# Kernel optimization log

Measured on AMD Instinct MI355X. Metric: run time of the kernel, lower is better.

Reference implementation:

```python
import jax, jax.numpy as jnp
import numpy as np

# Canonical DAG: L topological levels of N nodes each; every node in level l>0
# has K predecessors in level l-1, each edge carrying a scalar weight.
# Input nodes (level 0) take x columns directly (no activation), matching the
# torch module. Output = activations of the (sorted) last-level nodes.

B, N, K, L = 1024, 5000, 16, 10  # batch, nodes/level, fan-in, levels
NEG_SLOPE = 0.1                  # LeakyReLU(0.1) as in the module


def setup_inputs() -> dict:
    key = jax.random.key(0)
    k_x, k_s, k_w, k_b = jax.random.split(key, 4)
    x = jax.random.normal(k_x, (B, N), dtype=jnp.float32)
    # predecessor indices into the previous level, per level 1..L-1
    src_idx = jax.random.randint(k_s, (L - 1, N, K), 0, N)
    # scalar edge weights and node biases ~ N(0, 0.1), as in __init__
    weights = jax.random.normal(k_w, (L - 1, N, K), dtype=jnp.float32) * 0.1
    biases = jax.random.normal(k_b, (L - 1, N), dtype=jnp.float32) * 0.1
    return {"x": x, "src_idx": src_idx, "weights": weights, "biases": biases}


def reference(x, src_idx, weights, biases):
    b, n = x.shape
    k = src_idx.shape[-1]

    def level(act, params):
        s, w, bias = params  # s,w: [N,K], bias: [N]
        # gather predecessor activations: [B, N, K]
        gathered = jnp.take(act, s.reshape(-1), axis=1).reshape(b, n, k)
        # weighted sum over predecessors + bias, then LeakyReLU(0.1)
        pre = jnp.einsum('bnk,nk->bn', gathered, w) + bias
        return jax.nn.leaky_relu(pre, NEG_SLOPE), None

    out, _ = jax.lax.scan(level, x, (src_idx, weights, biases))
    return out  # [B, N] activations of output nodes (sorted order)
```

## Files before the change

kernel.cpp:

```cpp
#include <hip/hip_runtime.h>


#define TB 1024
#define TN 5000
#define TK 16
#define TLV 9
#define CPG 4
#define NG  (TB / CPG)
#define LT  1024
#define PEL (TN * TK)

typedef unsigned int u32;
typedef unsigned short u16;
typedef _Float16 h2 __attribute__((ext_vector_type(2)));

__device__ __forceinline__ h2 u2h(u32 v) { return __builtin_bit_cast(h2, v); }
__device__ __forceinline__ u32 h2u(h2 h) { return __builtin_bit_cast(u32, h); }
__device__ __forceinline__ u32 packf(float a, float b) {
    h2 h; h.x = (_Float16)a; h.y = (_Float16)b;
    return h2u(h);
}

__global__ __launch_bounds__(256) void k_pack(
    const int* __restrict__ idx, const float* __restrict__ w,
    u32* __restrict__ pe)
{
    const int j = blockIdx.x * 256 + threadIdx.x;
    if (j < TLV * TN * TK) {
        const u32 s = (u32)idx[j];
        h2 hw; hw.x = (_Float16)w[j]; hw.y = (_Float16)0.0f;
        pe[j] = (s * 8u) | (h2u(hw) << 16);
    }
}

__global__ __launch_bounds__(LT) void k_fused(
    const float* __restrict__ x,
    float* __restrict__ out,
    const u32* __restrict__ pe,
    const float* __restrict__ biases)
{
    __shared__ uint2 buf[2][TN];
    const int g = blockIdx.x;
    const int t = threadIdx.x;

    {
        const float* xp0 = x + (size_t)(g * CPG + 0) * TN;
        const float* xp1 = x + (size_t)(g * CPG + 1) * TN;
        const float* xp2 = x + (size_t)(g * CPG + 2) * TN;
        const float* xp3 = x + (size_t)(g * CPG + 3) * TN;
        for (int n = t; n < TN; n += LT) {
            uint2 v;
            v.x = packf(xp0[n], xp1[n]);
            v.y = packf(xp2[n], xp3[n]);
            buf[0][n] = v;
        }
    }
    __syncthreads();

    int cur = 0;
    for (int l = 0; l < TLV; ++l) {
        const u32*   ep_l = pe + (size_t)l * PEL;
        const float* b_l  = biases + (size_t)l * TN;
        const char*  base = reinterpret_cast<const char*>(buf[cur]);
        for (int n = t; n < TN; n += LT) {
            const uint4* ep = reinterpret_cast<const uint4*>(ep_l + (size_t)n * TK);
            const uint4 e0 = ep[0];
            const uint4 e1 = ep[1];
            const uint4 e2 = ep[2];
            const uint4 e3 = ep[3];
            const u32 es[TK] = {e0.x, e0.y, e0.z, e0.w,
                                e1.x, e1.y, e1.z, e1.w,
                                e2.x, e2.y, e2.z, e2.w,
                                e3.x, e3.y, e3.z, e3.w};

            const float bvf = b_l[n];
            h2 bb; bb.x = (_Float16)bvf; bb.y = (_Float16)bvf;
            h2 a01 = bb, a23 = bb;

            #pragma unroll
            for (int k = 0; k < TK; ++k) {
                const u32 e   = es[k];
                const u32 off = e & 0xffffu;
                const h2 w2 = u2h(__builtin_amdgcn_perm(e, e, 0x03020302u));
                const uint2 av = *reinterpret_cast<const uint2*>(base + off);
                a01 = w2 * u2h(av.x) + a01;
                a23 = w2 * u2h(av.y) + a23;
            }

            h2 tenth; tenth.x = (_Float16)0.1f; tenth.y = (_Float16)0.1f;
            a01 = __builtin_elementwise_max(a01, a01 * tenth);
            a23 = __builtin_elementwise_max(a23, a23 * tenth);

            uint2 r; r.x = h2u(a01); r.y = h2u(a23);
            buf[cur ^ 1][n] = r;
        }
        __syncthreads();
        cur ^= 1;
    }

    {
        float* op0 = out + (size_t)(g * CPG + 0) * TN;
        float* op1 = out + (size_t)(g * CPG + 1) * TN;
        float* op2 = out + (size_t)(g * CPG + 2) * TN;
        float* op3 = out + (size_t)(g * CPG + 3) * TN;
        for (int n = t; n < TN; n += LT) {
            const uint2 v = buf[cur][n];
            h2 h;
            h = u2h(v.x); op0[n] = (float)h.x; op1[n] = (float)h.y;
            h = u2h(v.y); op2[n] = (float)h.x; op3[n] = (float)h.y;
        }
    }
}

extern "C" void kernel_launch(void* const* d_in, const int* in_sizes, int n_in,
                              void* d_out, int out_size, void* d_ws, size_t ws_size,
                              hipStream_t stream)
{
    const float* x       = (const float*)d_in[0];
    const int*   src_idx = (const int*)  d_in[1];
    const float* weights = (const float*)d_in[2];
    const float* biases  = (const float*)d_in[3];
    float* out = (float*)d_out;

    u32* pe = (u32*)d_ws;

    {
        const int ne = TLV * TN * TK;
        hipLaunchKernelGGL(k_pack, dim3((ne + 255) / 256), dim3(256), 0, stream,
                           src_idx, weights, pe);
    }
    hipLaunchKernelGGL(k_fused, dim3(NG), dim3(LT), 0, stream,
                       x, out, pe, biases);
}
```

Measured before the change: 128.9 us.

## Duplicate activations into permuted LDS copy and reorder edges to cut bank conflicts

Each level's activations are now written twice into LDS: once in natural order and once in a permuted slot layout (sigma). The pack kernel assigns each node's 16 edges to the slot order k so that the address at iteration k tends to fall on a distinct bank phase across lanes, choosing between the two copies. The aim is to reduce LDS bank conflicts in the random gather, and the FMA now uses inline v_pk_fma_f16 with op_sel to read the weight straight from the packed word without a perm. In exchange, LDS use doubles (about 160KB per block) and every level does two stores per node.

```diff
diff --git a/kernel.cpp b/kernel.cpp
--- a/kernel.cpp
+++ b/kernel.cpp
@@ -10,6 +10,9 @@
 #define LT  1024
 #define PEL (TN * TK)
 
+#define SLOTS_A 5008
+#define SLOTS   10016
+
 typedef unsigned int u32;
 typedef unsigned short u16;
 typedef _Float16 h2 __attribute__((ext_vector_type(2)));
@@ -20,17 +23,61 @@
     h2 h; h.x = (_Float16)a; h.y = (_Float16)b;
     return h2u(h);
 }
+__device__ __forceinline__ u32 sigma(u32 n) { return (n & 15u) * 313u + (n >> 4); }
 
-__global__ __launch_bounds__(256) void k_pack(
+__global__ __launch_bounds__(256) void k_pack2(
     const int* __restrict__ idx, const float* __restrict__ w,
     u32* __restrict__ pe)
 {
-    const int j = blockIdx.x * 256 + threadIdx.x;
-    if (j < TLV * TN * TK) {
-        const u32 s = (u32)idx[j];
-        h2 hw; hw.x = (_Float16)w[j]; hw.y = (_Float16)0.0f;
-        pe[j] = (s * 8u) | (h2u(hw) << 16);
+    __shared__ u32 asg[256][17];
+    const int t = threadIdx.x;
+    const int j = blockIdx.x * 256 + t;
+    const int NT = TLV * TN;
+
+    if (j < NT) {
+        const u32 n  = (u32)(j % TN);
+        const int eb = j * TK;
+        const int4*   ip = reinterpret_cast<const int4*>(idx + eb);
+        const float4* wp = reinterpret_cast<const float4*>(w + eb);
+        const int4   i0 = ip[0], i1 = ip[1], i2 = ip[2], i3 = ip[3];
+        const float4 w0 = wp[0], w1 = wp[1], w2 = wp[2], w3 = wp[3];
+        const int   si[TK] = {i0.x,i0.y,i0.z,i0.w, i1.x,i1.y,i1.z,i1.w,
+                              i2.x,i2.y,i2.z,i2.w, i3.x,i3.y,i3.z,i3.w};
+        const float wv[TK] = {w0.x,w0.y,w0.z,w0.w, w1.x,w1.y,w1.z,w1.w,
+                              w2.x,w2.y,w2.z,w2.w, w3.x,w3.y,w3.z,w3.w};
+
+        u32 used = 0, pendmask = 0;
+        u32 valA[TK];
+        #pragma unroll
+        for (int k = 0; k < TK; ++k) {
+            const u32 s = (u32)si[k];
+            h2 hw; hw.x = (_Float16)wv[k]; hw.y = (_Float16)0.0f;
+            const u32 wb = h2u(hw) << 16;
+            const u32 offA = s;
+            const u32 offB = SLOTS_A + sigma(s);
+            valA[k] = offA | wb;
+            const u32 kA = (offA - n) & 15u;
+            const u32 kB = (offB - n) & 15u;
+            if (!((used >> kA) & 1u))      { used |= 1u << kA; asg[t][kA] = offA | wb; }
+            else if (!((used >> kB) & 1u)) { used |= 1u << kB; asg[t][kB] = offB | wb; }
+            else pendmask |= 1u << k;
+        }
+        #pragma unroll
+        for (int k = 0; k < TK; ++k) {
+            if ((pendmask >> k) & 1u) {
+                const u32 slot = (u32)__builtin_ctz(~used);
+                used |= 1u << slot;
+                asg[t][slot] = valA[k];
+            }
+        }
     }
+    __syncthreads();
+
+    const int jb    = blockIdx.x * 256;
+    const int nodeN = min(256, NT - jb);
+    const int elems = nodeN * TK;
+    for (int p = t; p < elems; p += 256)
+        pe[(size_t)jb * TK + p] = asg[p >> 4][p & 15];
 }
 
 __global__ __launch_bounds__(LT) void k_fused(
@@ -39,7 +86,7 @@
     const u32* __restrict__ pe,
     const float* __restrict__ biases)
 {
-    __shared__ uint2 buf[2][TN];
+    __shared__ uint2 buf[2][SLOTS];
     const int g = blockIdx.x;
     const int t = threadIdx.x;
 
@@ -53,6 +100,7 @@
             v.x = packf(xp0[n], xp1[n]);
             v.y = packf(xp2[n], xp3[n]);
             buf[0][n] = v;
+            buf[0][SLOTS_A + sigma((u32)n)] = v;
         }
     }
     __syncthreads();
@@ -62,6 +110,7 @@
         const u32*   ep_l = pe + (size_t)l * PEL;
         const float* b_l  = biases + (size_t)l * TN;
         const char*  base = reinterpret_cast<const char*>(buf[cur]);
+        uint2* wb = buf[cur ^ 1];
         for (int n = t; n < TN; n += LT) {
             const uint4* ep = reinterpret_cast<const uint4*>(ep_l + (size_t)n * TK);
             const uint4 e0 = ep[0];
@@ -74,25 +123,28 @@
                                 e3.x, e3.y, e3.z, e3.w};
 
             const float bvf = b_l[n];
-            h2 bb; bb.x = (_Float16)bvf; bb.y = (_Float16)bvf;
-            h2 a01 = bb, a23 = bb;
+            u32 a01 = packf(bvf, bvf);
+            u32 a23 = a01;
 
             #pragma unroll
             for (int k = 0; k < TK; ++k) {
                 const u32 e   = es[k];
-                const u32 off = e & 0xffffu;
-                const h2 w2 = u2h(__builtin_amdgcn_perm(e, e, 0x03020302u));
+                const u32 off = (e & 0xffffu) << 3;
                 const uint2 av = *reinterpret_cast<const uint2*>(base + off);
-                a01 = w2 * u2h(av.x) + a01;
-                a23 = w2 * u2h(av.y) + a23;
+                asm("v_pk_fma_f16 %0, %1, %2, %0 op_sel:[1,0,0] op_sel_hi:[1,1,1]"
+                    : "+v"(a01) : "v"(e), "v"(av.x));
+                asm("v_pk_fma_f16 %0, %1, %2, %0 op_sel:[1,0,0] op_sel_hi:[1,1,1]"
+                    : "+v"(a23) : "v"(e), "v"(av.y));
             }
 
+            h2 A = u2h(a01), Bv = u2h(a23);
             h2 tenth; tenth.x = (_Float16)0.1f; tenth.y = (_Float16)0.1f;
-            a01 = __builtin_elementwise_max(a01, a01 * tenth);
-            a23 = __builtin_elementwise_max(a23, a23 * tenth);
+            A  = __builtin_elementwise_max(A,  A  * tenth);
+            Bv = __builtin_elementwise_max(Bv, Bv * tenth);
 
-            uint2 r; r.x = h2u(a01); r.y = h2u(a23);
-            buf[cur ^ 1][n] = r;
+            uint2 r; r.x = h2u(A); r.y = h2u(Bv);
+            wb[n] = r;
+            wb[SLOTS_A + sigma((u32)n)] = r;
         }
         __syncthreads();
         cur ^= 1;
@@ -125,8 +177,8 @@
     u32* pe = (u32*)d_ws;
 
     {
-        const int ne = TLV * TN * TK;
-        hipLaunchKernelGGL(k_pack, dim3((ne + 255) / 256), dim3(256), 0, stream,
+        const int nn = TLV * TN;
+        hipLaunchKernelGGL(k_pack2, dim3((nn + 255) / 256), dim3(256), 0, stream,
                            src_idx, weights, pe);
     }
     hipLaunchKernelGGL(k_fused, dim3(NG), dim3(LT), 0, stream,
```

Result: no change. 130.3 us (+1.1%).

## Software-pipeline edge prefetch across nodes and levels with inline packed FMA

Applied to the files above, without the earlier changes.

Unrolls the per-level node loop into fixed iterations that use two register sets, so the edge descriptors and bias for the next node (and the first node of the next level) are loaded while the current node is computed. The bias is pre-packed to half2 in the pack kernel. Edge indices now encode a ping-pong slot offset into one flat LDS array, so no per-level base pointer is needed. Inline v_pk_fma_f16 with op_sel takes the weight straight from the high half of the edge word, replacing the perm. Register pressure rises with two prefetch sets at 1024 threads, and the hardcoded slot/iteration layout depends on N=5000.

```diff
diff --git a/kernel.cpp b/kernel.cpp
--- a/kernel.cpp
+++ b/kernel.cpp
@@ -9,6 +9,10 @@
 #define NG  (TB / CPG)
 #define LT  1024
 #define PEL (TN * TK)
+
+#define SLOTP 5056
+#define PSTRIDE (SLOTP * 8)
+#define WOFF_IT 8192
 
 typedef unsigned int u32;
 typedef unsigned short u16;
@@ -23,88 +27,129 @@
 
 __global__ __launch_bounds__(256) void k_pack(
     const int* __restrict__ idx, const float* __restrict__ w,
-    u32* __restrict__ pe)
+    const float* __restrict__ biases,
+    u32* __restrict__ pe, u32* __restrict__ b2)
 {
     const int j = blockIdx.x * 256 + threadIdx.x;
     if (j < TLV * TN * TK) {
+        const int l = j / (TN * TK);
         const u32 s = (u32)idx[j];
         h2 hw; hw.x = (_Float16)w[j]; hw.y = (_Float16)0.0f;
-        pe[j] = (s * 8u) | (h2u(hw) << 16);
+        pe[j] = ((u32)(l & 1) * (u32)SLOTP + s) | (h2u(hw) << 16);
+    }
+    if (j < TLV * TN) {
+        const float b = biases[j];
+        b2[j] = packf(b, b);
     }
 }
+
+
+#define PREF(S, LL, IT) do {                                                  \
+    const size_t _n = (size_t)(LL) * TN + (size_t)(t + (IT) * LT);            \
+    const uint4* _p = reinterpret_cast<const uint4*>(pe + _n * TK);           \
+    S##a = _p[0]; S##b = _p[1]; S##c = _p[2]; S##d = _p[3];                   \
+    S##i = b2[_n];                                                            \
+} while (0)
+
+#define EDGE(EV) do {                                                         \
+    const u32 _e   = (EV);                                                    \
+    const u32 _off = (_e & 0xffffu) << 3;              \
+    const uint2 _av = *reinterpret_cast<const uint2*>(lds + _off);            \
+    asm("v_pk_fma_f16 %0, %1, %2, %0 op_sel:[1,0,0] op_sel_hi:[1,1,1]"        \
+        : "+v"(a01) : "v"(_e), "v"(_av.x));                                   \
+    asm("v_pk_fma_f16 %0, %1, %2, %0 op_sel:[1,0,0] op_sel_hi:[1,1,1]"        \
+        : "+v"(a23) : "v"(_e), "v"(_av.y));                                   \
+} while (0)
+
+#define COMP(S, WBASE, IT) do {                                               \
+    u32 a01 = S##i, a23 = S##i;                      \
+    EDGE(S##a.x); EDGE(S##a.y); EDGE(S##a.z); EDGE(S##a.w);                   \
+    EDGE(S##b.x); EDGE(S##b.y); EDGE(S##b.z); EDGE(S##b.w);                   \
+    EDGE(S##c.x); EDGE(S##c.y); EDGE(S##c.z); EDGE(S##c.w);                   \
+    EDGE(S##d.x); EDGE(S##d.y); EDGE(S##d.z); EDGE(S##d.w);                   \
+    h2 A = u2h(a01), Bv = u2h(a23);                                           \
+    h2 tenth; tenth.x = (_Float16)0.1f; tenth.y = (_Float16)0.1f;             \
+    A  = __builtin_elementwise_max(A,  A  * tenth);                           \
+    Bv = __builtin_elementwise_max(Bv, Bv * tenth);                           \
+    uint2 _r; _r.x = h2u(A); _r.y = h2u(Bv);                                  \
+    *reinterpret_cast<uint2*>(lds + (WBASE) + (IT) * WOFF_IT) = _r;           \
+} while (0)
+
+#define LVL(LL, S0, S1, WBASE, LAST) do {                                     \
+    PREF(S1, (LL), 1); COMP(S0, WBASE, 0);                                    \
+    PREF(S0, (LL), 2); COMP(S1, WBASE, 1);                                    \
+    PREF(S1, (LL), 3); COMP(S0, WBASE, 2);                                    \
+    if (t4) PREF(S0, (LL), 4);                                                \
+    COMP(S1, WBASE, 3);                                                       \
+    if (!(LAST)) PREF(S1, (LL) + 1, 0);                                       \
+    if (t4) COMP(S0, WBASE, 4);                                               \
+    __syncthreads();                                                          \
+} while (0)
 
 __global__ __launch_bounds__(LT) void k_fused(
     const float* __restrict__ x,
     float* __restrict__ out,
     const u32* __restrict__ pe,
-    const float* __restrict__ biases)
+    const u32* __restrict__ b2)
 {
-    __shared__ uint2 buf[2][TN];
+    __shared__ char lds[2 * PSTRIDE];
     const int g = blockIdx.x;
     const int t = threadIdx.x;
+    const bool t4 = t < (TN - 4 * LT);
+    const u32 woO = (u32)t * 8u;
+    const u32 woE = (u32)(SLOTP + t) * 8u;
+
+    uint4 Pa, Pb, Pc, Pd; u32 Pi;
+    uint4 Qa, Qb, Qc, Qd; u32 Qi;
+
+    PREF(P, 0, 0);
 
     {
         const float* xp0 = x + (size_t)(g * CPG + 0) * TN;
         const float* xp1 = x + (size_t)(g * CPG + 1) * TN;
         const float* xp2 = x + (size_t)(g * CPG + 2) * TN;
         const float* xp3 = x + (size_t)(g * CPG + 3) * TN;
-        for (int n = t; n < TN; n += LT) {
+        #pragma unroll
+        for (int it = 0; it < 4; ++it) {
+            const int n = t + it * LT;
             uint2 v;
             v.x = packf(xp0[n], xp1[n]);
             v.y = packf(xp2[n], xp3[n]);
-            buf[0][n] = v;
+            *reinterpret_cast<uint2*>(lds + woO + it * WOFF_IT) = v;
+        }
+        if (t4) {
+            const int n = t + 4 * LT;
+            uint2 v;
+            v.x = packf(xp0[n], xp1[n]);
+            v.y = packf(xp2[n], xp3[n]);
+            *reinterpret_cast<uint2*>(lds + woO + 4 * WOFF_IT) = v;
         }
     }
     __syncthreads();
 
-    int cur = 0;
-    for (int l = 0; l < TLV; ++l) {
-        const u32*   ep_l = pe + (size_t)l * PEL;
-        const float* b_l  = biases + (size_t)l * TN;
-        const char*  base = reinterpret_cast<const char*>(buf[cur]);
-        for (int n = t; n < TN; n += LT) {
-            const uint4* ep = reinterpret_cast<const uint4*>(ep_l + (size_t)n * TK);
-            const uint4 e0 = ep[0];
-            const uint4 e1 = ep[1];
-            const uint4 e2 = ep[2];
-            const uint4 e3 = ep[3];
-            const u32 es[TK] = {e0.x, e0.y, e0.z, e0.w,
-                                e1.x, e1.y, e1.z, e1.w,
-                                e2.x, e2.y, e2.z, e2.w,
-                                e3.x, e3.y, e3.z, e3.w};
-
-            const float bvf = b_l[n];
-            h2 bb; bb.x = (_Float16)bvf; bb.y = (_Float16)bvf;
-            h2 a01 = bb, a23 = bb;
-
-            #pragma unroll
-            for (int k = 0; k < TK; ++k) {
-                const u32 e   = es[k];
-                const u32 off = e & 0xffffu;
-                const h2 w2 = u2h(__builtin_amdgcn_perm(e, e, 0x03020302u));
-                const uint2 av = *reinterpret_cast<const uint2*>(base + off);
-                a01 = w2 * u2h(av.x) + a01;
-                a23 = w2 * u2h(av.y) + a23;
-            }
-
-            h2 tenth; tenth.x = (_Float16)0.1f; tenth.y = (_Float16)0.1f;
-            a01 = __builtin_elementwise_max(a01, a01 * tenth);
-            a23 = __builtin_elementwise_max(a23, a23 * tenth);
-
-            uint2 r; r.x = h2u(a01); r.y = h2u(a23);
-            buf[cur ^ 1][n] = r;
-        }
-        __syncthreads();
-        cur ^= 1;
+    #pragma unroll 1
+    for (int lp = 0; lp < 4; ++lp) {
+        LVL(2 * lp,     P, Q, woE, false);
+        LVL(2 * lp + 1, Q, P, woO, false);
     }
+    LVL(8, P, Q, woE, true);
 
     {
         float* op0 = out + (size_t)(g * CPG + 0) * TN;
         float* op1 = out + (size_t)(g * CPG + 1) * TN;
         float* op2 = out + (size_t)(g * CPG + 2) * TN;
         float* op3 = out + (size_t)(g * CPG + 3) * TN;
-        for (int n = t; n < TN; n += LT) {
-            const uint2 v = buf[cur][n];
+        #pragma unroll
+        for (int it = 0; it < 4; ++it) {
+            const int n = t + it * LT;
+            const uint2 v = *reinterpret_cast<const uint2*>(lds + woE + it * WOFF_IT);
+            h2 h;
+            h = u2h(v.x); op0[n] = (float)h.x; op1[n] = (float)h.y;
+            h = u2h(v.y); op2[n] = (float)h.x; op3[n] = (float)h.y;
+        }
+        if (t4) {
+            const int n = t + 4 * LT;
+            const uint2 v = *reinterpret_cast<const uint2*>(lds + woE + 4 * WOFF_IT);
             h2 h;
             h = u2h(v.x); op0[n] = (float)h.x; op1[n] = (float)h.y;
             h = u2h(v.y); op2[n] = (float)h.x; op3[n] = (float)h.y;
@@ -123,12 +168,13 @@
     float* out = (float*)d_out;
 
     u32* pe = (u32*)d_ws;
+    u32* b2 = pe + (size_t)TLV * TN * TK;
 
     {
         const int ne = TLV * TN * TK;
         hipLaunchKernelGGL(k_pack, dim3((ne + 255) / 256), dim3(256), 0, stream,
-                           src_idx, weights, pe);
+                           src_idx, weights, biases, pe, b2);
     }
     hipLaunchKernelGGL(k_fused, dim3(NG), dim3(LT), 0, stream,
-                       x, out, pe, biases);
+                       x, out, pe, b2);
 }
```

New measurement: 135.0 us. 4.7% more time.

## Halve batch columns per block to shrink LDS and fold ping-pong offsets into packed edges

Applied to the files above, without the earlier changes.

Each block now carries two batch columns per node instead of four, which halves the LDS footprint and doubles the grid; launch bounds request higher occupancy. The ping-pong buffer offset is folded into the packed edge word at pack time, so the inner loop does a single 4-byte LDS gather plus one inline-asm packed FMA using op_sel to pick the weight half directly. Biases are pre-packed as fp16 pairs. The trade-off is that the edge stream is read twice as many times overall, since each block reuses it across fewer columns.

```diff
diff --git a/kernel.cpp b/kernel.cpp
--- a/kernel.cpp
+++ b/kernel.cpp
@@ -5,10 +5,13 @@
 #define TN 5000
 #define TK 16
 #define TLV 9
-#define CPG 4
+#define CPG 2
 #define NG  (TB / CPG)
 #define LT  1024
 #define PEL (TN * TK)
+
+#define SLOTP 5056
+#define PBYTES (SLOTP * 4)
 
 typedef unsigned int u32;
 typedef unsigned short u16;
@@ -23,45 +26,46 @@
 
 __global__ __launch_bounds__(256) void k_pack(
     const int* __restrict__ idx, const float* __restrict__ w,
-    u32* __restrict__ pe)
+    const float* __restrict__ biases,
+    u32* __restrict__ pe, u32* __restrict__ b2)
 {
     const int j = blockIdx.x * 256 + threadIdx.x;
     if (j < TLV * TN * TK) {
+        const int l = j / (TN * TK);
         const u32 s = (u32)idx[j];
         h2 hw; hw.x = (_Float16)w[j]; hw.y = (_Float16)0.0f;
-        pe[j] = (s * 8u) | (h2u(hw) << 16);
+        pe[j] = ((u32)(l & 1) * (u32)PBYTES + s * 4u) | (h2u(hw) << 16);
+    }
+    if (j < TLV * TN) {
+        const float b = biases[j];
+        b2[j] = packf(b, b);
     }
 }
 
-__global__ __launch_bounds__(LT) void k_fused(
+__global__ __launch_bounds__(LT, 8) void k_fused(
     const float* __restrict__ x,
     float* __restrict__ out,
     const u32* __restrict__ pe,
-    const float* __restrict__ biases)
+    const u32* __restrict__ b2)
 {
-    __shared__ uint2 buf[2][TN];
+    __shared__ u32 buf[2 * SLOTP];
+    const char* lds = reinterpret_cast<const char*>(buf);
     const int g = blockIdx.x;
     const int t = threadIdx.x;
 
     {
         const float* xp0 = x + (size_t)(g * CPG + 0) * TN;
         const float* xp1 = x + (size_t)(g * CPG + 1) * TN;
-        const float* xp2 = x + (size_t)(g * CPG + 2) * TN;
-        const float* xp3 = x + (size_t)(g * CPG + 3) * TN;
-        for (int n = t; n < TN; n += LT) {
-            uint2 v;
-            v.x = packf(xp0[n], xp1[n]);
-            v.y = packf(xp2[n], xp3[n]);
-            buf[0][n] = v;
-        }
+        for (int n = t; n < TN; n += LT)
+            buf[n] = packf(xp0[n], xp1[n]);
     }
     __syncthreads();
 
     int cur = 0;
     for (int l = 0; l < TLV; ++l) {
-        const u32*   ep_l = pe + (size_t)l * PEL;
-        const float* b_l  = biases + (size_t)l * TN;
-        const char*  base = reinterpret_cast<const char*>(buf[cur]);
+        const u32* ep_l = pe + (size_t)l * PEL;
+        const u32* b_l  = b2 + (size_t)l * TN;
+        u32* wb = buf + (cur ^ 1) * SLOTP;
         for (int n = t; n < TN; n += LT) {
             const uint4* ep = reinterpret_cast<const uint4*>(ep_l + (size_t)n * TK);
             const uint4 e0 = ep[0];
@@ -73,26 +77,21 @@
                                 e2.x, e2.y, e2.z, e2.w,
                                 e3.x, e3.y, e3.z, e3.w};
 
-            const float bvf = b_l[n];
-            h2 bb; bb.x = (_Float16)bvf; bb.y = (_Float16)bvf;
-            h2 a01 = bb, a23 = bb;
+            u32 acc = b_l[n];
 
             #pragma unroll
             for (int k = 0; k < TK; ++k) {
                 const u32 e   = es[k];
                 const u32 off = e & 0xffffu;
-                const h2 w2 = u2h(__builtin_amdgcn_perm(e, e, 0x03020302u));
-                const uint2 av = *reinterpret_cast<const uint2*>(base + off);
-                a01 = w2 * u2h(av.x) + a01;
-                a23 = w2 * u2h(av.y) + a23;
+                const u32 av  = *reinterpret_cast<const u32*>(lds + off);
+                asm("v_pk_fma_f16 %0, %1, %2, %0 op_sel:[1,0,0] op_sel_hi:[1,1,1]"
+                    : "+v"(acc) : "v"(e), "v"(av));
             }
 
+            h2 A = u2h(acc);
             h2 tenth; tenth.x = (_Float16)0.1f; tenth.y = (_Float16)0.1f;
-            a01 = __builtin_elementwise_max(a01, a01 * tenth);
-            a23 = __builtin_elementwise_max(a23, a23 * tenth);
-
-            uint2 r; r.x = h2u(a01); r.y = h2u(a23);
-            buf[cur ^ 1][n] = r;
+            A = __builtin_elementwise_max(A, A * tenth);
+            wb[n] = h2u(A);
         }
         __syncthreads();
         cur ^= 1;
@@ -101,13 +100,10 @@
     {
         float* op0 = out + (size_t)(g * CPG + 0) * TN;
         float* op1 = out + (size_t)(g * CPG + 1) * TN;
-        float* op2 = out + (size_t)(g * CPG + 2) * TN;
-        float* op3 = out + (size_t)(g * CPG + 3) * TN;
         for (int n = t; n < TN; n += LT) {
-            const uint2 v = buf[cur][n];
-            h2 h;
-            h = u2h(v.x); op0[n] = (float)h.x; op1[n] = (float)h.y;
-            h = u2h(v.y); op2[n] = (float)h.x; op3[n] = (float)h.y;
+            const h2 h = u2h(buf[SLOTP + n]);
+            op0[n] = (float)h.x;
+            op1[n] = (float)h.y;
         }
     }
 }
@@ -123,12 +119,13 @@
     float* out = (float*)d_out;
 
     u32* pe = (u32*)d_ws;
+    u32* b2 = pe + (size_t)TLV * TN * TK;
 
     {
         const int ne = TLV * TN * TK;
         hipLaunchKernelGGL(k_pack, dim3((ne + 255) / 256), dim3(256), 0, stream,
-                           src_idx, weights, pe);
+                           src_idx, weights, biases, pe, b2);
     }
     hipLaunchKernelGGL(k_fused, dim3(NG), dim3(LT), 0, stream,
-                       x, out, pe, biases);
+                       x, out, pe, b2);
 }
```

Result: slower. 165.6 us (+28.5%).
